# Kernel optimization log

Measured on AMD Instinct MI355X. Metric: run time of the kernel, lower is better.

The kernel has to match this reference:

```python
import jax, jax.numpy as jnp
import numpy as np

D_MODEL = 1024
N_HEAD = 16
D_K = D_MODEL // N_HEAD


def setup_inputs() -> dict:
    key = jax.random.key(0)
    ks = jax.random.split(key, 11)
    B, S = 2, 2048
    std = 1.0 / np.sqrt(D_MODEL)
    inp = {
        "Q": jax.random.normal(ks[0], (B, S, D_MODEL), jnp.float32),
        "K": jax.random.normal(ks[1], (B, S, D_MODEL), jnp.float32),
        "V": jax.random.normal(ks[2], (B, S, D_MODEL), jnp.float32),
        "Wq": jax.random.normal(ks[3], (D_MODEL, D_MODEL), jnp.float32) * std,
        "bq": jnp.zeros((D_MODEL,), jnp.float32),
        "Wk": jax.random.normal(ks[4], (D_MODEL, D_MODEL), jnp.float32) * std,
        "bk": jnp.zeros((D_MODEL,), jnp.float32),
        "Wv": jax.random.normal(ks[5], (D_MODEL, D_MODEL), jnp.float32) * std,
        "bv": jnp.zeros((D_MODEL,), jnp.float32),
        "Wo": jax.random.normal(ks[6], (D_MODEL, D_MODEL), jnp.float32) * std,
        "bo": jnp.zeros((D_MODEL,), jnp.float32),
    }
    return inp


def _split_heads(x):
    # [B, S, D] -> [B, H, S, d_k]
    B, S, _ = x.shape
    return x.reshape(B, S, N_HEAD, D_K).transpose(0, 2, 1, 3)


def reference(Q, K, V, Wq, bq, Wk, bk, Wv, bv, Wo, bo):
    q = _split_heads(Q @ Wq.T + bq)   # [B,H,S,dk]
    k = _split_heads(K @ Wk.T + bk)
    v = _split_heads(V @ Wv.T + bv)
    scale = 1.0 / jnp.sqrt(jnp.float32(D_K))
    scores = jnp.einsum("bhqd,bhkd->bhqk", q, k) * scale
    attn = jax.nn.softmax(scores, axis=-1)
    ctx = jnp.einsum("bhqk,bhkd->bhqd", attn, v)  # [B,H,S,dk]
    B, H, S, dk = ctx.shape
    ctx = ctx.transpose(0, 2, 1, 3).reshape(B, S, H * dk)
    return ctx @ Wo.T + bo
```

## Files before the change

### kernel.cpp

```cpp
#include <hip/hip_runtime.h>
#include <hip/hip_bf16.h>
#include <cstdint>
#include <cstddef>
#include <cmath>

typedef __attribute__((ext_vector_type(8))) short short8;
typedef __attribute__((ext_vector_type(4))) short short4_t;
typedef __attribute__((ext_vector_type(4))) float f32x4;
typedef __attribute__((ext_vector_type(16))) float f32x16;

constexpr int B_ = 2, S_ = 2048, H_ = 16, DK_ = 64, DM_ = 1024;

__device__ inline unsigned short f2bf(float x) {
  union { float f; unsigned u; } c; c.f = x;
  unsigned r = c.u + 0x7FFF + ((c.u >> 16) & 1);
  return (unsigned short)(r >> 16);
}

__device__ inline float ex2(float x) {
#if __has_builtin(__builtin_amdgcn_exp2f)
  return __builtin_amdgcn_exp2f(x);
#else
  return exp2f(x);
#endif
}

__device__ inline unsigned pkbf(float lo, float hi) {
  unsigned u;
  asm("v_cvt_pk_bf16_f32 %0, %1, %2" : "=v"(u) : "v"(lo), "v"(hi));
  return u;
}

__device__ inline f32x4 mfma16(short8 a, short8 b, f32x4 c) {
  return __builtin_amdgcn_mfma_f32_16x16x32_bf16(a, b, c, 0, 0, 0);
}
__device__ inline f32x16 mfma32(short8 a, short8 b, f32x16 c) {
  return __builtin_amdgcn_mfma_f32_32x32x16_bf16(a, b, c, 0, 0, 0);
}

__device__ inline void glds16(const unsigned short* g, unsigned short* l) {
  __builtin_amdgcn_global_load_lds(
      (const __attribute__((address_space(1))) unsigned int*)g,
      (__attribute__((address_space(3))) unsigned int*)l, 16, 0, 0);
}

__global__ __launch_bounds__(256) void cvt_all(
    const float* __restrict__ Q, const float* __restrict__ K,
    const float* __restrict__ V, const float* __restrict__ Wq,
    const float* __restrict__ Wk, const float* __restrict__ Wv,
    const float* __restrict__ Wo, unsigned short* __restrict__ Qb,
    unsigned short* __restrict__ Kb, unsigned short* __restrict__ Vb,
    unsigned short* __restrict__ Wqb, unsigned short* __restrict__ Wkb,
    unsigned short* __restrict__ Wvb, unsigned short* __restrict__ Wob) {
  int bid = blockIdx.x;
  const float* in; unsigned short* out; int off;
  if (bid < 4096)       { in = Q;  out = Qb;  off = bid; }
  else if (bid < 8192)  { in = K;  out = Kb;  off = bid - 4096; }
  else if (bid < 12288) { in = V;  out = Vb;  off = bid - 8192; }
  else if (bid < 13312) { in = Wq; out = Wqb; off = bid - 12288; }
  else if (bid < 14336) { in = Wk; out = Wkb; off = bid - 13312; }
  else if (bid < 15360) { in = Wv; out = Wvb; off = bid - 14336; }
  else                  { in = Wo; out = Wob; off = bid - 15360; }
  int i = off * 256 + threadIdx.x;
  float4 f = ((const float4*)in)[i];
  uint2 o;
  o.x = pkbf(f.x, f.y);
  o.y = pkbf(f.z, f.w);
  ((uint2*)out)[i] = o;
}

__device__ inline void store_out(float* p, float v) { *p = v; }
__device__ inline void store_out(unsigned short* p, float v) { *p = f2bf(v); }

template <typename OUT_T>
__device__ inline void gemm_body(const unsigned short* __restrict__ A,
                                 const unsigned short* __restrict__ Bw,
                                 const float* __restrict__ bias,
                                 OUT_T* __restrict__ C, float cscale,
                                 int bm, int bn) {
  constexpr int Kd = 1024, Nd = 1024;
  __shared__ unsigned short As[128][64];
  __shared__ unsigned short Bs[64][64];

  const int tid = threadIdx.x;
  const int lane = tid & 63, wave = tid >> 6;
  const int li = lane & 15, lg = lane >> 4;
  const int wm = wave >> 1, wn = wave & 1;

  const f32x4 zero4 = {0.f, 0.f, 0.f, 0.f};
  f32x4 acc[4][2];
#pragma unroll
  for (int i = 0; i < 4; i++)
#pragma unroll
    for (int j = 0; j < 2; j++) acc[i][j] = zero4;

  const int stg_row = tid >> 3;
  const int stg_col = (tid & 7) * 8;
  const unsigned short* Ag = A + (size_t)(bm * 128 + stg_row) * Kd + stg_col;
  const unsigned short* Bg = Bw + (size_t)(bn * 64 + stg_row) * Kd + stg_col;

  for (int kt = 0; kt < Kd; kt += 64) {
#pragma unroll
    for (int i = 0; i < 4; i++)
      glds16(Ag + (size_t)(i * 32) * Kd + kt, &As[i * 32 + stg_row][stg_col]);
#pragma unroll
    for (int i = 0; i < 2; i++)
      glds16(Bg + (size_t)(i * 32) * Kd + kt, &Bs[i * 32 + stg_row][stg_col]);
    __syncthreads();

    short8 af[4][2], bf[2][2];
#pragma unroll
    for (int kb = 0; kb < 2; kb++) {
#pragma unroll
      for (int i = 0; i < 4; i++)
        af[i][kb] = *(const short8*)&As[wm * 64 + i * 16 + li][kb * 32 + lg * 8];
#pragma unroll
      for (int j = 0; j < 2; j++)
        bf[j][kb] = *(const short8*)&Bs[wn * 32 + j * 16 + li][kb * 32 + lg * 8];
    }
#pragma unroll
    for (int kb = 0; kb < 2; kb++)
#pragma unroll
      for (int i = 0; i < 4; i++)
#pragma unroll
        for (int j = 0; j < 2; j++)
          acc[i][j] = mfma16(af[i][kb], bf[j][kb], acc[i][j]);
    __syncthreads();
  }

#pragma unroll
  for (int j = 0; j < 2; j++) {
    int col = bn * 64 + wn * 32 + j * 16 + li;
    float bv = bias[col];
#pragma unroll
    for (int i = 0; i < 4; i++) {
      int row0 = bm * 128 + wm * 64 + i * 16 + lg * 4;
#pragma unroll
      for (int r = 0; r < 4; r++)
        store_out(&C[(size_t)(row0 + r) * Nd + col], (acc[i][j][r] + bv) * cscale);
    }
  }
}

__global__ __launch_bounds__(256) void gemm_qkv(
    const unsigned short* __restrict__ Aq, const unsigned short* __restrict__ Ak,
    const unsigned short* __restrict__ Av, const unsigned short* __restrict__ Bq,
    const unsigned short* __restrict__ Bk, const unsigned short* __restrict__ Bv,
    const float* __restrict__ bq, const float* __restrict__ bk,
    const float* __restrict__ bv, unsigned short* __restrict__ Cq,
    unsigned short* __restrict__ Ck, unsigned short* __restrict__ Cv,
    float qscale) {
  const int n = blockIdx.x;
  const int xcd = n & 7, m = n >> 3;
  const int z = m >> 6, idx = m & 63;
  const int bm = xcd * 4 + (idx >> 4), bn = idx & 15;
  const unsigned short* A = z == 0 ? Aq : z == 1 ? Ak : Av;
  const unsigned short* Bw = z == 0 ? Bq : z == 1 ? Bk : Bv;
  const float* bi = z == 0 ? bq : z == 1 ? bk : bv;
  unsigned short* C = z == 0 ? Cq : z == 1 ? Ck : Cv;
  gemm_body(A, Bw, bi, C, z == 0 ? qscale : 1.0f, bm, bn);
}

__global__ __launch_bounds__(256) void gemm_out(
    const unsigned short* __restrict__ A, const unsigned short* __restrict__ Bw,
    const float* __restrict__ bias, float* __restrict__ C) {
  const int n = blockIdx.x;
  const int xcd = n & 7, m = n >> 3;
  const int bm = xcd * 4 + (m >> 4), bn = m & 15;
  gemm_body(A, Bw, bias, C, 1.0f, bm, bn);
}

__global__ __launch_bounds__(256) void attn_fwd(
    const unsigned short* __restrict__ q, const unsigned short* __restrict__ k,
    const unsigned short* __restrict__ v, unsigned short* __restrict__ ctx) {
  __shared__ unsigned short Ks[2][64][64];
  __shared__ unsigned short Vt[64][64];

  const int tid = threadIdx.x;
  const int lane = tid & 63, wave = tid >> 6;
  const int l31 = lane & 31, h = lane >> 5;
  const int n = blockIdx.x;
  const int xcd = n & 7, m = n >> 3;
  const int bh = xcd * 4 + (m & 3);
  const int qt = m >> 2;
  const int b = bh >> 4, hd = bh & 15;

  const int qrow = qt * 128 + wave * 32 + l31;
  const unsigned short* qg = q + (size_t)(b * S_ + qrow) * DM_ + hd * DK_;
  short8 qf[4];
#pragma unroll
  for (int t = 0; t < 4; t++) qf[t] = *(const short8*)(qg + t * 16 + h * 8);

  f32x16 po[2];
#pragma unroll
  for (int db = 0; db < 2; db++)
#pragma unroll
    for (int r = 0; r < 16; r++) po[db][r] = 0.f;
  float m_i = -1e30f, l_i = 0.f;

  const int srow = tid >> 3;
  const int sc = tid & 7;
  const int scs = (sc ^ (srow & 7)) * 8;
  const unsigned short* kg = k + (size_t)(b * S_) * DM_ + hd * DK_;

  const int vm = tid & 31;
  const int vkey2 = vm * 2;
  const int vd0 = (tid >> 5) * 8;
  const unsigned short* vg = v + (size_t)(b * S_) * DM_ + hd * DK_;

  const int NT = S_ / 64;

  glds16(kg + (size_t)srow * DM_ + scs, &Ks[0][srow][sc * 8]);
  glds16(kg + (size_t)(32 + srow) * DM_ + scs, &Ks[0][32 + srow][sc * 8]);
  short8 t0, t1;
  {
    const unsigned short* vp = vg + (size_t)vkey2 * DM_ + vd0;
    t0 = *(const short8*)(vp);
    t1 = *(const short8*)(vp + DM_);
  }

  for (int kt = 0; kt < NT; kt++) {
    const int buf = kt & 1;
    asm volatile("s_waitcnt vmcnt(0)" ::: "memory");
    __builtin_amdgcn_sched_barrier(0);
    __builtin_amdgcn_s_barrier();
    __builtin_amdgcn_sched_barrier(0);

#pragma unroll
    for (int j = 0; j < 8; j++) {
      unsigned w = (unsigned)(unsigned short)t0[j] |
                   ((unsigned)(unsigned short)t1[j] << 16);
      int slot = (vm >> 2) ^ j;
      *(unsigned*)&Vt[vd0 + j][slot * 8 + (vkey2 & 7)] = w;
    }

    if (kt + 1 < NT) {
      const unsigned short* kgt = kg + (size_t)((kt + 1) * 64) * DM_;
      glds16(kgt + (size_t)srow * DM_ + scs, &Ks[buf ^ 1][srow][sc * 8]);
      glds16(kgt + (size_t)(32 + srow) * DM_ + scs, &Ks[buf ^ 1][32 + srow][sc * 8]);
      const unsigned short* vp = vg + (size_t)((kt + 1) * 64 + vkey2) * DM_ + vd0;
      t0 = *(const short8*)(vp);
      t1 = *(const short8*)(vp + DM_);
    }

    asm volatile("s_waitcnt lgkmcnt(0)" ::: "memory");
    __builtin_amdgcn_sched_barrier(0);
    __builtin_amdgcn_s_barrier();
    __builtin_amdgcn_sched_barrier(0);

    f32x16 sacc[2];
#pragma unroll
    for (int kb = 0; kb < 2; kb++)
#pragma unroll
      for (int r = 0; r < 16; r++) sacc[kb][r] = 0.f;
#pragma unroll
    for (int t = 0; t < 4; t++) {
      const int slot = ((t << 1) | h) ^ (l31 & 7);
#pragma unroll
      for (int kb = 0; kb < 2; kb++) {
        short8 kf = *(const short8*)&Ks[buf][kb * 32 + l31][slot * 8];
        sacc[kb] = mfma32(kf, qf[t], sacc[kb]);
      }
    }

    float mx;
    {
      float a = -1e30f, c = -1e30f;
#pragma unroll
      for (int r = 0; r < 16; r += 2) {
        a = fmaxf(a, fmaxf(sacc[0][r], sacc[0][r + 1]));
        c = fmaxf(c, fmaxf(sacc[1][r], sacc[1][r + 1]));
      }
      mx = fmaxf(a, c);
    }
    mx = fmaxf(mx, __shfl_xor(mx, 32));

    if (!__all(mx - m_i <= 8.0f)) {
      float mn = fmaxf(m_i, mx);
      float al = ex2(m_i - mn);
      m_i = mn;
      l_i *= al;
#pragma unroll
      for (int db = 0; db < 2; db++)
#pragma unroll
        for (int r = 0; r < 16; r++) po[db][r] *= al;
    }

    float s0 = 0.f, s1 = 0.f, s2 = 0.f, s3 = 0.f;
#pragma unroll
    for (int kb = 0; kb < 2; kb++)
#pragma unroll
      for (int r = 0; r < 16; r += 4) {
        float p0 = ex2(sacc[kb][r] - m_i);
        float p1 = ex2(sacc[kb][r + 1] - m_i);
        float p2 = ex2(sacc[kb][r + 2] - m_i);
        float p3 = ex2(sacc[kb][r + 3] - m_i);
        sacc[kb][r] = p0; sacc[kb][r + 1] = p1;
        sacc[kb][r + 2] = p2; sacc[kb][r + 3] = p3;
        s0 += p0; s1 += p1; s2 += p2; s3 += p3;
      }
    float sum = (s0 + s1) + (s2 + s3);
    sum += __shfl_xor(sum, 32);
    l_i += sum;

    unsigned u[2][4][2];
#pragma unroll
    for (int kb = 0; kb < 2; kb++)
#pragma unroll
      for (int qd = 0; qd < 4; qd++) {
        u[kb][qd][0] = pkbf(sacc[kb][4 * qd], sacc[kb][4 * qd + 1]);
        u[kb][qd][1] = pkbf(sacc[kb][4 * qd + 2], sacc[kb][4 * qd + 3]);
      }

#pragma unroll
    for (int t = 0; t < 4; t++) {
      const int kb = t >> 1, qe = (t & 1) * 2;
      unsigned X0 = u[kb][qe][0], X1 = u[kb][qe][1];
      unsigned Y0 = u[kb][qe + 1][0], Y1 = u[kb][qe + 1][1];
      unsigned sX0 = __shfl_xor(X0, 32), sX1 = __shfl_xor(X1, 32);
      unsigned sY0 = __shfl_xor(Y0, 32), sY1 = __shfl_xor(Y1, 32);
      union { unsigned w[4]; short8 v8; } fr;
      fr.w[0] = h ? sY0 : X0;
      fr.w[1] = h ? sY1 : X1;
      fr.w[2] = h ? Y0 : sX0;
      fr.w[3] = h ? Y1 : sX1;
      const int slot = ((t << 1) | h) ^ (l31 & 7);
#pragma unroll
      for (int db = 0; db < 2; db++) {
        short8 vf = *(const short8*)&Vt[db * 32 + l31][slot * 8];
        po[db] = mfma32(vf, fr.v8, po[db]);
      }
    }
  }

  float rl = 1.0f / l_i;
  unsigned short* cg = ctx + (size_t)(b * S_ + qrow) * DM_ + hd * DK_;
#pragma unroll
  for (int db = 0; db < 2; db++)
#pragma unroll
    for (int rq = 0; rq < 4; rq++) {
      uint2 w2;
      w2.x = pkbf(po[db][4 * rq] * rl, po[db][4 * rq + 1] * rl);
      w2.y = pkbf(po[db][4 * rq + 2] * rl, po[db][4 * rq + 3] * rl);
      *(uint2*)(cg + db * 32 + 8 * rq + 4 * h) = w2;
    }
}

extern "C" void kernel_launch(void* const* d_in, const int* in_sizes, int n_in,
                              void* d_out, int out_size, void* d_ws, size_t ws_size,
                              hipStream_t stream) {
  const float* Q  = (const float*)d_in[0];
  const float* Kx = (const float*)d_in[1];
  const float* V  = (const float*)d_in[2];
  const float* Wq = (const float*)d_in[3];
  const float* bq = (const float*)d_in[4];
  const float* Wk = (const float*)d_in[5];
  const float* bk = (const float*)d_in[6];
  const float* Wv = (const float*)d_in[7];
  const float* bv = (const float*)d_in[8];
  const float* Wo = (const float*)d_in[9];
  const float* bo = (const float*)d_in[10];
  float* out = (float*)d_out;

  char* ws = (char*)d_ws;
  const size_t MB = 1ull << 20;
  unsigned short* Qb  = (unsigned short*)(ws + 0 * MB);
  unsigned short* Kb  = (unsigned short*)(ws + 8 * MB);
  unsigned short* Vb  = (unsigned short*)(ws + 16 * MB);
  unsigned short* Wqb = (unsigned short*)(ws + 24 * MB);
  unsigned short* Wkb = (unsigned short*)(ws + 26 * MB);
  unsigned short* Wvb = (unsigned short*)(ws + 28 * MB);
  unsigned short* Wob = (unsigned short*)(ws + 30 * MB);
  unsigned short* qp  = (unsigned short*)(ws + 32 * MB);
  unsigned short* kp  = (unsigned short*)(ws + 40 * MB);
  unsigned short* vp  = (unsigned short*)(ws + 48 * MB);
  unsigned short* cx  = (unsigned short*)(ws + 56 * MB);

  cvt_all<<<16384, 256, 0, stream>>>(Q, Kx, V, Wq, Wk, Wv, Wo,
                                     Qb, Kb, Vb, Wqb, Wkb, Wvb, Wob);

  gemm_qkv<<<1536, 256, 0, stream>>>(
      Qb, Kb, Vb, Wqb, Wkb, Wvb, bq, bk, bv, qp, kp, vp, 0.18033688f);

  attn_fwd<<<512, 256, 0, stream>>>(qp, kp, vp, cx);

  gemm_out<<<512, 256, 0, stream>>>(cx, Wob, bo, out);
}
```

Before: 148.2 us.

## Widen attention key tile to 128, double-buffer V transpose, drop one barrier per tile

The attention kernel now processes 128 keys per iteration instead of 64. V is double-buffered in LDS with a wider swizzle, so each tile needs only one block barrier instead of two, and the K prefetch is issued after that barrier. The loop is unrolled by two with register ping-pong for the V prefetch, QK MFMAs run at raised wave priority, and softmax/PV is interleaved per key block. The cost is more LDS (64KB) and more registers, with launch_bounds asking for 2 blocks per CU.

```diff
diff --git a/kernel.cpp b/kernel.cpp
--- a/kernel.cpp
+++ b/kernel.cpp
@@ -170,11 +170,143 @@
   gemm_body(A, Bw, bias, C, 1.0f, bm, bn);
 }
 
-__global__ __launch_bounds__(256) void attn_fwd(
+struct V4 { short8 v[4]; };
+
+__device__ __forceinline__ void attn_tile_step(
+    int kt, int buf, int NT,
+    const unsigned short* kg, const unsigned short* vg,
+    unsigned short* KsAll, unsigned short* VtAll,
+    int srow, int sc, int scs, int key2, int dq,
+    const short8* qf, int l31, int h,
+    V4& vc, V4& vn, f32x16* po, float& m_i, float& l_i) {
+  unsigned short* KsB = KsAll + buf * (128 * 64);
+  unsigned short* VtB = VtAll + buf * (64 * 128);
+  unsigned short* KsO = KsAll + (buf ^ 1) * (128 * 64);
+
+  asm volatile("s_waitcnt vmcnt(0)" ::: "memory");
+  __builtin_amdgcn_sched_barrier(0);
+
+#pragma unroll
+  for (int j = 0; j < 16; j++) {
+    const int half = j >> 3, jj = j & 7;
+    unsigned w = (unsigned)(unsigned short)vc.v[half][jj] |
+                 ((unsigned)(unsigned short)vc.v[2 + half][jj] << 16);
+    const int slot = (key2 >> 3) ^ j;
+    *(unsigned*)&VtB[(dq * 16 + j) * 128 + slot * 8 + (key2 & 7)] = w;
+  }
+
+  if (kt + 1 < NT) {
+    const unsigned short* vp =
+        vg + (size_t)((kt + 1) * 128 + key2) * DM_ + dq * 16;
+    vn.v[0] = *(const short8*)(vp);
+    vn.v[1] = *(const short8*)(vp + 8);
+    vn.v[2] = *(const short8*)(vp + DM_);
+    vn.v[3] = *(const short8*)(vp + DM_ + 8);
+  }
+
+  asm volatile("s_waitcnt lgkmcnt(0)" ::: "memory");
+  __builtin_amdgcn_sched_barrier(0);
+  __builtin_amdgcn_s_barrier();
+  __builtin_amdgcn_sched_barrier(0);
+
+  if (kt + 1 < NT) {
+    const unsigned short* kgt = kg + (size_t)((kt + 1) * 128) * DM_;
+#pragma unroll
+    for (int i = 0; i < 4; i++)
+      glds16(kgt + (size_t)(i * 32 + srow) * DM_ + scs,
+             &KsO[(i * 32 + srow) * 64 + sc * 8]);
+  }
+  __builtin_amdgcn_sched_barrier(0);
+
+  f32x16 sacc[4];
+#pragma unroll
+  for (int kb = 0; kb < 4; kb++)
+#pragma unroll
+    for (int r = 0; r < 16; r++) sacc[kb][r] = 0.f;
+
+  __builtin_amdgcn_s_setprio(1);
+#pragma unroll
+  for (int tq = 0; tq < 4; tq++) {
+    const int sl = ((((tq << 1) | h) ^ (l31 & 7))) * 8;
+#pragma unroll
+    for (int kb = 0; kb < 4; kb++) {
+      short8 kf = *(const short8*)&KsB[(kb * 32 + l31) * 64 + sl];
+      sacc[kb] = mfma32(kf, qf[tq], sacc[kb]);
+    }
+  }
+  __builtin_amdgcn_s_setprio(0);
+
+  float mx = -1e30f;
+#pragma unroll
+  for (int kb = 0; kb < 4; kb++)
+#pragma unroll
+    for (int r = 0; r < 16; r += 4)
+      mx = fmaxf(mx, fmaxf(fmaxf(sacc[kb][r], sacc[kb][r + 1]),
+                           fmaxf(sacc[kb][r + 2], sacc[kb][r + 3])));
+  mx = fmaxf(mx, __shfl_xor(mx, 32));
+
+  if (!__all(mx - m_i <= 8.0f)) {
+    float mn = fmaxf(m_i, mx);
+    float al = ex2(m_i - mn);
+    m_i = mn;
+    l_i *= al;
+#pragma unroll
+    for (int db = 0; db < 2; db++)
+#pragma unroll
+      for (int r = 0; r < 16; r++) po[db][r] *= al;
+  }
+
+  float s0 = 0.f, s1 = 0.f, s2 = 0.f, s3 = 0.f;
+#pragma unroll
+  for (int kb = 0; kb < 4; kb++) {
+#pragma unroll
+    for (int r = 0; r < 16; r += 4) {
+      float p0 = ex2(sacc[kb][r] - m_i);
+      float p1 = ex2(sacc[kb][r + 1] - m_i);
+      float p2 = ex2(sacc[kb][r + 2] - m_i);
+      float p3 = ex2(sacc[kb][r + 3] - m_i);
+      sacc[kb][r] = p0; sacc[kb][r + 1] = p1;
+      sacc[kb][r + 2] = p2; sacc[kb][r + 3] = p3;
+      s0 += p0; s1 += p1; s2 += p2; s3 += p3;
+    }
+    unsigned u[4][2];
+#pragma unroll
+    for (int qd = 0; qd < 4; qd++) {
+      u[qd][0] = pkbf(sacc[kb][4 * qd], sacc[kb][4 * qd + 1]);
+      u[qd][1] = pkbf(sacc[kb][4 * qd + 2], sacc[kb][4 * qd + 3]);
+    }
+#pragma unroll
+    for (int tt = 0; tt < 2; tt++) {
+      const int tp = 2 * kb + tt, qe = tt * 2;
+      unsigned X0 = u[qe][0], X1 = u[qe][1];
+      unsigned Y0 = u[qe + 1][0], Y1 = u[qe + 1][1];
+      unsigned sX0 = __shfl_xor(X0, 32), sX1 = __shfl_xor(X1, 32);
+      unsigned sY0 = __shfl_xor(Y0, 32), sY1 = __shfl_xor(Y1, 32);
+      union { unsigned w[4]; short8 v8; } fr;
+      fr.w[0] = h ? sY0 : X0;
+      fr.w[1] = h ? sY1 : X1;
+      fr.w[2] = h ? Y0 : sX0;
+      fr.w[3] = h ? Y1 : sX1;
+      const int slbase = (tp << 1) | h;
+#pragma unroll
+      for (int db = 0; db < 2; db++) {
+        const int row = db * 32 + l31;
+        short8 vf = *(const short8*)
+            &VtB[row * 128 + (slbase ^ (l31 & 15)) * 8];
+        po[db] = mfma32(vf, fr.v8, po[db]);
+      }
+    }
+  }
+  float sum = (s0 + s1) + (s2 + s3);
+  sum += __shfl_xor(sum, 32);
+  l_i += sum;
+}
+
+__global__ __launch_bounds__(256, 2) void attn_fwd(
     const unsigned short* __restrict__ q, const unsigned short* __restrict__ k,
     const unsigned short* __restrict__ v, unsigned short* __restrict__ ctx) {
-  __shared__ unsigned short Ks[2][64][64];
-  __shared__ unsigned short Vt[64][64];
+  __shared__ unsigned short Ks[2][128][64];
+  __shared__ unsigned short Vt[2][64][128];
 
   const int tid = threadIdx.x;
   const int lane = tid & 63, wave = tid >> 6;
@@ -198,139 +330,35 @@
     for (int r = 0; r < 16; r++) po[db][r] = 0.f;
   float m_i = -1e30f, l_i = 0.f;
 
-  const int srow = tid >> 3;
-  const int sc = tid & 7;
+  const int srow = tid >> 3, sc = tid & 7;
   const int scs = (sc ^ (srow & 7)) * 8;
   const unsigned short* kg = k + (size_t)(b * S_) * DM_ + hd * DK_;
 
-  const int vm = tid & 31;
-  const int vkey2 = vm * 2;
-  const int vd0 = (tid >> 5) * 8;
+  const int key2 = (tid & 63) * 2, dq = tid >> 6;
   const unsigned short* vg = v + (size_t)(b * S_) * DM_ + hd * DK_;
 
-  const int NT = S_ / 64;
-
-  glds16(kg + (size_t)srow * DM_ + scs, &Ks[0][srow][sc * 8]);
-  glds16(kg + (size_t)(32 + srow) * DM_ + scs, &Ks[0][32 + srow][sc * 8]);
-  short8 t0, t1;
+  const int NT = S_ / 128;
+
+#pragma unroll
+  for (int i = 0; i < 4; i++)
+    glds16(kg + (size_t)(i * 32 + srow) * DM_ + scs,
+           &Ks[0][i * 32 + srow][sc * 8]);
+  V4 va, vb;
   {
-    const unsigned short* vp = vg + (size_t)vkey2 * DM_ + vd0;
-    t0 = *(const short8*)(vp);
-    t1 = *(const short8*)(vp + DM_);
-  }
-
-  for (int kt = 0; kt < NT; kt++) {
-    const int buf = kt & 1;
-    asm volatile("s_waitcnt vmcnt(0)" ::: "memory");
-    __builtin_amdgcn_sched_barrier(0);
-    __builtin_amdgcn_s_barrier();
-    __builtin_amdgcn_sched_barrier(0);
-
-#pragma unroll
-    for (int j = 0; j < 8; j++) {
-      unsigned w = (unsigned)(unsigned short)t0[j] |
-                   ((unsigned)(unsigned short)t1[j] << 16);
-      int slot = (vm >> 2) ^ j;
-      *(unsigned*)&Vt[vd0 + j][slot * 8 + (vkey2 & 7)] = w;
-    }
-
-    if (kt + 1 < NT) {
-      const unsigned short* kgt = kg + (size_t)((kt + 1) * 64) * DM_;
-      glds16(kgt + (size_t)srow * DM_ + scs, &Ks[buf ^ 1][srow][sc * 8]);
-      glds16(kgt + (size_t)(32 + srow) * DM_ + scs, &Ks[buf ^ 1][32 + srow][sc * 8]);
-      const unsigned short* vp = vg + (size_t)((kt + 1) * 64 + vkey2) * DM_ + vd0;
-      t0 = *(const short8*)(vp);
-      t1 = *(const short8*)(vp + DM_);
-    }
-
-    asm volatile("s_waitcnt lgkmcnt(0)" ::: "memory");
-    __builtin_amdgcn_sched_barrier(0);
-    __builtin_amdgcn_s_barrier();
-    __builtin_amdgcn_sched_barrier(0);
-
-    f32x16 sacc[2];
-#pragma unroll
-    for (int kb = 0; kb < 2; kb++)
-#pragma unroll
-      for (int r = 0; r < 16; r++) sacc[kb][r] = 0.f;
-#pragma unroll
-    for (int t = 0; t < 4; t++) {
-      const int slot = ((t << 1) | h) ^ (l31 & 7);
-#pragma unroll
-      for (int kb = 0; kb < 2; kb++) {
-        short8 kf = *(const short8*)&Ks[buf][kb * 32 + l31][slot * 8];
-        sacc[kb] = mfma32(kf, qf[t], sacc[kb]);
-      }
-    }
-
-    float mx;
-    {
-      float a = -1e30f, c = -1e30f;
-#pragma unroll
-      for (int r = 0; r < 16; r += 2) {
-        a = fmaxf(a, fmaxf(sacc[0][r], sacc[0][r + 1]));
-        c = fmaxf(c, fmaxf(sacc[1][r], sacc[1][r + 1]));
-      }
-      mx = fmaxf(a, c);
-    }
-    mx = fmaxf(mx, __shfl_xor(mx, 32));
-
-    if (!__all(mx - m_i <= 8.0f)) {
-      float mn = fmaxf(m_i, mx);
-      float al = ex2(m_i - mn);
-      m_i = mn;
-      l_i *= al;
-#pragma unroll
-      for (int db = 0; db < 2; db++)
-#pragma unroll
-        for (int r = 0; r < 16; r++) po[db][r] *= al;
-    }
-
-    float s0 = 0.f, s1 = 0.f, s2 = 0.f, s3 = 0.f;
-#pragma unroll
-    for (int kb = 0; kb < 2; kb++)
-#pragma unroll
-      for (int r = 0; r < 16; r += 4) {
-        float p0 = ex2(sacc[kb][r] - m_i);
-        float p1 = ex2(sacc[kb][r + 1] - m_i);
-        float p2 = ex2(sacc[kb][r + 2] - m_i);
-        float p3 = ex2(sacc[kb][r + 3] - m_i);
-        sacc[kb][r] = p0; sacc[kb][r + 1] = p1;
-        sacc[kb][r + 2] = p2; sacc[kb][r + 3] = p3;
-        s0 += p0; s1 += p1; s2 += p2; s3 += p3;
-      }
-    float sum = (s0 + s1) + (s2 + s3);
-    sum += __shfl_xor(sum, 32);
-    l_i += sum;
-
-    unsigned u[2][4][2];
-#pragma unroll
-    for (int kb = 0; kb < 2; kb++)
-#pragma unroll
-      for (int qd = 0; qd < 4; qd++) {
-        u[kb][qd][0] = pkbf(sacc[kb][4 * qd], sacc[kb][4 * qd + 1]);
-        u[kb][qd][1] = pkbf(sacc[kb][4 * qd + 2], sacc[kb][4 * qd + 3]);
-      }
-
-#pragma unroll
-    for (int t = 0; t < 4; t++) {
-      const int kb = t >> 1, qe = (t & 1) * 2;
-      unsigned X0 = u[kb][qe][0], X1 = u[kb][qe][1];
-      unsigned Y0 = u[kb][qe + 1][0], Y1 = u[kb][qe + 1][1];
-      unsigned sX0 = __shfl_xor(X0, 32), sX1 = __shfl_xor(X1, 32);
-      unsigned sY0 = __shfl_xor(Y0, 32), sY1 = __shfl_xor(Y1, 32);
-      union { unsigned w[4]; short8 v8; } fr;
-      fr.w[0] = h ? sY0 : X0;
-      fr.w[1] = h ? sY1 : X1;
-      fr.w[2] = h ? Y0 : sX0;
-      fr.w[3] = h ? Y1 : sX1;
-      const int slot = ((t << 1) | h) ^ (l31 & 7);
-#pragma unroll
-      for (int db = 0; db < 2; db++) {
-        short8 vf = *(const short8*)&Vt[db * 32 + l31][slot * 8];
-        po[db] = mfma32(vf, fr.v8, po[db]);
-      }
-    }
+    const unsigned short* vp = vg + (size_t)key2 * DM_ + dq * 16;
+    va.v[0] = *(const short8*)(vp);
+    va.v[1] = *(const short8*)(vp + 8);
+    va.v[2] = *(const short8*)(vp + DM_);
+    va.v[3] = *(const short8*)(vp + DM_ + 8);
+  }
+
+  unsigned short* KsAll = &Ks[0][0][0];
+  unsigned short* VtAll = &Vt[0][0][0];
+  for (int it = 0; it < NT; it += 2) {
+    attn_tile_step(it, 0, NT, kg, vg, KsAll, VtAll, srow, sc, scs, key2, dq,
+                   qf, l31, h, va, vb, po, m_i, l_i);
+    attn_tile_step(it + 1, 1, NT, kg, vg, KsAll, VtAll, srow, sc, scs, key2,
+                   dq, qf, l31, h, vb, va, po, m_i, l_i);
   }
 
   float rl = 1.0f / l_i;
```

Result: faster. 138.1 us (-6.8%).
